# Optimization experiments

Hardware: AMD Instinct MI355X
Metric: run time of the kernel (lower is better)

## Reference

```python
import jax, jax.numpy as jnp
import numpy as np

N_FEATURES = 2048


def setup_inputs() -> dict:
    key = jax.random.key(0)
    kx, kd, kl, ku = jax.random.split(key, 4)
    x = jax.random.normal(kx, (32, 1024, N_FEATURES), dtype=jnp.float32)
    # torch initializes these params to zeros; use small random values so
    # gradients/flow are non-degenerate while keeping M diagonally dominant.
    d = 0.1 * jax.random.normal(kd, (N_FEATURES,), dtype=jnp.float32)
    l = 0.1 * jax.random.normal(kl, (N_FEATURES - 1,), dtype=jnp.float32)
    u = 0.1 * jax.random.normal(ku, (N_FEATURES - 1,), dtype=jnp.float32)
    return {"x": x, "d": d, "l": l, "u": u}


def reference(x, d, l, u):
    # Build tridiagonal matrix M (faithful to the torch dense construction)
    diag = jax.nn.softplus(d) + 2.0          # [n]
    off_l = jnp.tanh(l)                       # [n-1], subdiagonal
    off_u = jnp.tanh(u)                       # [n-1], superdiagonal
    M = jnp.diag(diag) + jnp.diag(off_l, -1) + jnp.diag(off_u, 1)  # [n, n]
    # Solve M @ y_t = x^T for each batch: x [B, S, n] -> x_t [B, n, S]
    x_t = jnp.swapaxes(x, -2, -1)
    y_t = jnp.linalg.solve(M, x_t)            # M broadcasts over batch
    return jnp.swapaxes(y_t, -2, -1)          # [B, S, n]
```

## Files before the change

### kernel.cpp

```cpp
#include <hip/hip_runtime.h>
#include <math.h>

#define NF 2048
#define ROWS (32 * 1024)
#define CELLS (NF / 4)
#define PHASES 8
#define NBLOCKS 4096
#define BLKTHREADS 512

typedef float f32x4 __attribute__((ext_vector_type(4)));

__device__ __forceinline__ float dpp_up1(float v, float oldv) {
  return __int_as_float(__builtin_amdgcn_update_dpp(
      __float_as_int(oldv), __float_as_int(v), 0x138, 0xF, 0xF, false));
}
__device__ __forceinline__ float dpp_dn1(float v, float oldv) {
  return __int_as_float(__builtin_amdgcn_update_dpp(
      __float_as_int(oldv), __float_as_int(v), 0x130, 0xF, 0xF, false));
}
__device__ __forceinline__ float bcast_lane(float v, int lane) {
  return __int_as_float(__builtin_amdgcn_readlane(__float_as_int(v), lane));
}

__global__ __launch_bounds__(256) void precompute_kernel(
    const float* __restrict__ d, const float* __restrict__ l,
    const float* __restrict__ u, float* __restrict__ wsg,
    float* __restrict__ wsc, float* __restrict__ wsib) {
  __shared__ float diag_s[NF], tl_s[NF], tu_s[NF], b_s[NF];
  const int tid = threadIdx.x;

  for (int i = tid; i < NF; i += 256) {
    float dv = d[i];
    float sp = (dv > 20.f) ? dv : log1pf(expf(dv));
    diag_s[i] = sp + 2.f;
    tl_s[i] = (i < NF - 1) ? tanhf(l[i]) : 0.f;
    tu_s[i] = (i < NF - 1) ? tanhf(u[i]) : 0.f;
  }
  __syncthreads();

  if (tid < 64) {
    const int lane = tid;
    float T00 = 1.f, T01 = 0.f, T10 = 0.f, T11 = 1.f;
#pragma unroll 1
    for (int j = 0; j < 32; ++j) {
      int i = lane * 32 + j;
      float a = diag_s[i];
      float b = (i > 0) ? -tl_s[i - 1] * tu_s[i - 1] : 0.f;
      float n00 = a * T00 + b * T10;
      float n01 = a * T01 + b * T11;
      T10 = T00; T11 = T01; T00 = n00; T01 = n01;
      float s = 1.f / (fabsf(T00) + fabsf(T01) + 1e-30f);
      T00 *= s; T01 *= s; T10 *= s; T11 *= s;
    }
    for (int ofs = 1; ofs < 64; ofs <<= 1) {
      float U00 = __shfl_up(T00, ofs, 64);
      float U01 = __shfl_up(T01, ofs, 64);
      float U10 = __shfl_up(T10, ofs, 64);
      float U11 = __shfl_up(T11, ofs, 64);
      if (lane >= ofs) {
        float n00 = T00 * U00 + T01 * U10;
        float n01 = T00 * U01 + T01 * U11;
        float n10 = T10 * U00 + T11 * U10;
        float n11 = T10 * U01 + T11 * U11;
        T00 = n00; T01 = n01; T10 = n10; T11 = n11;
        float s = 1.f / (fabsf(T00) + fabsf(T01) + 1e-30f);
        T00 *= s; T01 *= s; T10 *= s; T11 *= s;
      }
    }
    float p1 = __shfl_up(T00, 1, 64);
    float p2 = __shfl_up(T10, 1, 64);
    float bp = (lane == 0) ? 1.f : p1 / p2;
#pragma unroll 1
    for (int j = 0; j < 32; ++j) {
      int i = lane * 32 + j;
      float km1 = (i > 0) ? tl_s[i - 1] * tu_s[i - 1] : 0.f;
      float bv = diag_s[i] - km1 / bp;
      b_s[i] = bv;
      bp = bv;
    }
  }
  __syncthreads();

  for (int i = tid; i < NF; i += 256) {
    float invb = 1.f / b_s[i];
    wsg[i] = (i > 0) ? -tl_s[i - 1] / b_s[i - 1] : 0.f;
    wsc[i] = (i < NF - 1) ? -tu_s[i] * invb : 0.f;
    wsib[i] = invb;
  }
}

__global__ __launch_bounds__(BLKTHREADS, 8) void solve_kernel(
    const float* __restrict__ x, const float* __restrict__ wsg,
    const float* __restrict__ wsc, const float* __restrict__ wsib,
    float* __restrict__ y) {
  __shared__ float4 g_s[CELLS], c_s[CELLS], ib_s[CELLS];

  const int lane = threadIdx.x & 63;
  const unsigned row = (blockIdx.x * BLKTHREADS + threadIdx.x) >> 6;
  const unsigned o = row * (NF / 4) + lane;
  const float4* xb = (const float4*)x;
  float4* yb = (float4*)y;

  float4 v[PHASES];
#pragma unroll
  for (int t = 0; t < PHASES; ++t) v[t] = xb[o + t * 64];
  __builtin_amdgcn_sched_barrier(0);

  for (int t = threadIdx.x; t < CELLS; t += BLKTHREADS) {
    g_s[t] = ((const float4*)wsg)[t];
    c_s[t] = ((const float4*)wsc)[t];
    ib_s[t] = ((const float4*)wsib)[t];
  }
  __syncthreads();

  const float4* gs = &g_s[lane];
  const float4* cs = &c_s[lane];
  const float4* ibs = &ib_s[lane];

  {
    float ct = 0.f;
#pragma unroll
    for (int t = 0; t < PHASES; ++t) {
      float4 g = gs[t * 64];
      float4 dv = v[t];
      dv.y = fmaf(g.y, dv.x, dv.y);
      dv.z = fmaf(g.z, dv.y, dv.z);
      dv.w = fmaf(g.w, dv.z, dv.w);
      float A = g.x * g.y * g.z * g.w;
      float A2 = A * dpp_up1(A, 1.f);
      float B = fmaf(A, dpp_up1(dv.w, 0.f), dv.w);
      B = fmaf(A2, ct, B);
      float vin = dpp_up1(B, ct);
      ct = bcast_lane(B, 63);
      float p = g.x;
      dv.x = fmaf(p, vin, dv.x);
      p *= g.y; dv.y = fmaf(p, vin, dv.y);
      p *= g.z; dv.z = fmaf(p, vin, dv.z);
      p *= g.w; dv.w = fmaf(p, vin, dv.w);
      v[t] = dv;
    }
  }

  {
    float ct = 0.f;
#pragma unroll
    for (int t = PHASES - 1; t >= 0; --t) {
      float4 c = cs[t * 64];
      float4 ib = ibs[t * 64];
      float4 dv = v[t];
      float4 w;
      w.w = ib.w * dv.w;
      w.z = fmaf(c.z, w.w, ib.z * dv.z);
      w.y = fmaf(c.y, w.z, ib.y * dv.y);
      w.x = fmaf(c.x, w.y, ib.x * dv.x);
      float A = c.x * c.y * c.z * c.w;
      float A2 = A * dpp_dn1(A, 1.f);
      float B = fmaf(A, dpp_dn1(w.x, 0.f), w.x);
      B = fmaf(A2, ct, B);
      float vin = dpp_dn1(B, ct);
      ct = bcast_lane(B, 0);
      float p = c.w;
      w.w = fmaf(p, vin, w.w);
      p *= c.z; w.z = fmaf(p, vin, w.z);
      p *= c.y; w.y = fmaf(p, vin, w.y);
      p *= c.x; w.x = fmaf(p, vin, w.x);
      __builtin_nontemporal_store(*(const f32x4*)&w, (f32x4*)&yb[o + t * 64]);
    }
  }
}

extern "C" void kernel_launch(void* const* d_in, const int* in_sizes, int n_in,
                              void* d_out, int out_size, void* d_ws,
                              size_t ws_size, hipStream_t stream) {
  const float* x = (const float*)d_in[0];
  const float* d = (const float*)d_in[1];
  const float* l = (const float*)d_in[2];
  const float* u = (const float*)d_in[3];
  float* out = (float*)d_out;

  float* wsg = (float*)d_ws;
  float* wsc = wsg + NF;
  float* wsib = wsc + NF;

  precompute_kernel<<<1, 256, 0, stream>>>(d, l, u, wsg, wsc, wsib);
  solve_kernel<<<NBLOCKS, BLKTHREADS, 0, stream>>>(x, wsg, wsc, wsib, out);
}
```

Before: 112.3 us.

## Split each row's tridiagonal solve across two wavefronts with LDS carry exchange

```diff
diff --git a/kernel.cpp b/kernel.cpp
--- a/kernel.cpp
+++ b/kernel.cpp
@@ -4,8 +4,8 @@
 #define NF 2048
 #define ROWS (32 * 1024)
 #define CELLS (NF / 4)
-#define PHASES 8
-#define NBLOCKS 4096
+#define HPH 4
+#define NBLOCKS 8192
 #define BLKTHREADS 512
 
 typedef float f32x4 __attribute__((ext_vector_type(4)));
@@ -94,17 +94,20 @@
     const float* __restrict__ wsc, const float* __restrict__ wsib,
     float* __restrict__ y) {
   __shared__ float4 g_s[CELLS], c_s[CELLS], ib_s[CELLS];
+  __shared__ float cf_s[4], cb_s[4];
 
   const int lane = threadIdx.x & 63;
-  const unsigned row = (blockIdx.x * BLKTHREADS + threadIdx.x) >> 6;
-  const unsigned o = row * (NF / 4) + lane;
+  const int wid = threadIdx.x >> 6;
+  const int rowinblk = wid >> 1;
+  const int half = wid & 1;
+  const unsigned row = blockIdx.x * 4u + rowinblk;
+  const unsigned o = row * (unsigned)CELLS + half * (CELLS / 2) + lane;
   const float4* xb = (const float4*)x;
   float4* yb = (float4*)y;
 
-  float4 v[PHASES];
+  float4 v[HPH];
 #pragma unroll
-  for (int t = 0; t < PHASES; ++t) v[t] = xb[o + t * 64];
-  __builtin_amdgcn_sched_barrier(0);
+  for (int t = 0; t < HPH; ++t) v[t] = xb[o + t * 64];
 
   for (int t = threadIdx.x; t < CELLS; t += BLKTHREADS) {
     g_s[t] = ((const float4*)wsg)[t];
@@ -113,14 +116,15 @@
   }
   __syncthreads();
 
-  const float4* gs = &g_s[lane];
-  const float4* cs = &c_s[lane];
-  const float4* ibs = &ib_s[lane];
-
+  const float4* gs = &g_s[half * (CELLS / 2) + lane];
+  const float4* cs = &c_s[half * (CELLS / 2) + lane];
+  const float4* ibs = &ib_s[half * (CELLS / 2) + lane];
+
+  float A0s = 0.f, B0s = 0.f;
   {
     float ct = 0.f;
 #pragma unroll
-    for (int t = 0; t < PHASES; ++t) {
+    for (int t = 0; t < HPH; ++t) {
       float4 g = gs[t * 64];
       float4 dv = v[t];
       dv.y = fmaf(g.y, dv.x, dv.y);
@@ -129,22 +133,45 @@
       float A = g.x * g.y * g.z * g.w;
       float A2 = A * dpp_up1(A, 1.f);
       float B = fmaf(A, dpp_up1(dv.w, 0.f), dv.w);
-      B = fmaf(A2, ct, B);
-      float vin = dpp_up1(B, ct);
-      ct = bcast_lane(B, 63);
-      float p = g.x;
-      dv.x = fmaf(p, vin, dv.x);
-      p *= g.y; dv.y = fmaf(p, vin, dv.y);
-      p *= g.z; dv.z = fmaf(p, vin, dv.z);
-      p *= g.w; dv.w = fmaf(p, vin, dv.w);
+      if (half == 0 || t > 0) {
+        B = fmaf(A2, ct, B);
+        float vin = dpp_up1(B, ct);
+        float ctn = bcast_lane(B, 63);
+        float p = g.x;
+        dv.x = fmaf(p, vin, dv.x);
+        p *= g.y; dv.y = fmaf(p, vin, dv.y);
+        p *= g.z; dv.z = fmaf(p, vin, dv.z);
+        p *= g.w; dv.w = fmaf(p, vin, dv.w);
+        ct = ctn;
+      } else {
+        A0s = A2;
+        B0s = B;
+        ct = bcast_lane(B, 63);
+      }
       v[t] = dv;
     }
-  }
-
+    if (half == 0 && lane == 0) cf_s[rowinblk] = ct;
+  }
+  __syncthreads();
+  if (half == 1) {
+    float ctin = cf_s[rowinblk];
+    float4 g = gs[0];
+    float4 dv = v[0];
+    float B = fmaf(A0s, ctin, B0s);
+    float vin = dpp_up1(B, ctin);
+    float p = g.x;
+    dv.x = fmaf(p, vin, dv.x);
+    p *= g.y; dv.y = fmaf(p, vin, dv.y);
+    p *= g.z; dv.z = fmaf(p, vin, dv.z);
+    p *= g.w; dv.w = fmaf(p, vin, dv.w);
+    v[0] = dv;
+  }
+
+  float A3s = 0.f, B3s = 0.f;
   {
     float ct = 0.f;
 #pragma unroll
-    for (int t = PHASES - 1; t >= 0; --t) {
+    for (int t = HPH - 1; t >= 0; --t) {
       float4 c = cs[t * 64];
       float4 ib = ibs[t * 64];
       float4 dv = v[t];
@@ -156,16 +183,41 @@
       float A = c.x * c.y * c.z * c.w;
       float A2 = A * dpp_dn1(A, 1.f);
       float B = fmaf(A, dpp_dn1(w.x, 0.f), w.x);
-      B = fmaf(A2, ct, B);
-      float vin = dpp_dn1(B, ct);
-      ct = bcast_lane(B, 0);
-      float p = c.w;
-      w.w = fmaf(p, vin, w.w);
-      p *= c.z; w.z = fmaf(p, vin, w.z);
-      p *= c.y; w.y = fmaf(p, vin, w.y);
-      p *= c.x; w.x = fmaf(p, vin, w.x);
-      __builtin_nontemporal_store(*(const f32x4*)&w, (f32x4*)&yb[o + t * 64]);
-    }
+      if (half == 1 || t < HPH - 1) {
+        B = fmaf(A2, ct, B);
+        float vin = dpp_dn1(B, ct);
+        float ctn = bcast_lane(B, 0);
+        float p = c.w;
+        w.w = fmaf(p, vin, w.w);
+        p *= c.z; w.z = fmaf(p, vin, w.z);
+        p *= c.y; w.y = fmaf(p, vin, w.y);
+        p *= c.x; w.x = fmaf(p, vin, w.x);
+        __builtin_nontemporal_store(*(const f32x4*)&w,
+                                    (f32x4*)&yb[o + t * 64]);
+        ct = ctn;
+      } else {
+        A3s = A2;
+        B3s = B;
+        ct = bcast_lane(B, 0);
+        v[HPH - 1] = w;
+      }
+    }
+    if (half == 1 && lane == 0) cb_s[rowinblk] = ct;
+  }
+  __syncthreads();
+  if (half == 0) {
+    float ctin = cb_s[rowinblk];
+    float4 c = cs[(HPH - 1) * 64];
+    float4 w = v[HPH - 1];
+    float B = fmaf(A3s, ctin, B3s);
+    float vin = dpp_dn1(B, ctin);
+    float p = c.w;
+    w.w = fmaf(p, vin, w.w);
+    p *= c.z; w.z = fmaf(p, vin, w.z);
+    p *= c.y; w.y = fmaf(p, vin, w.y);
+    p *= c.x; w.x = fmaf(p, vin, w.x);
+    __builtin_nontemporal_store(*(const f32x4*)&w,
+                                (f32x4*)&yb[o + (HPH - 1) * 64]);
   }
 }
 
```

Measured after the change: 110.5 us. No clear change (-1.5%).
